# Kernel tuning notes

Hardware: AMD Instinct MI355X
Metric: run time of the kernel (lower is better)

## Reference

```python
import jax, jax.numpy as jnp
import numpy as np

W = 1022      # window_length (fft_length) -> 512 rfft bins
HOP = 256     # hop_length
F = 64        # frames
ORDER = 5     # butterworth order
WN = 0.5      # normalized cutoff (cutoff = fs/4)

# ---- Butterworth lowpass design (scipy.signal.butter equivalent, numpy only) ----
def _butter_lowpass(order, wn):
    m = np.arange(-order + 1, order, 2)
    p = -np.exp(1j * np.pi * m / (2 * order))        # analog prototype poles
    k = 1.0
    fs = 2.0
    warped = 2 * fs * np.tan(np.pi * wn / fs)        # pre-warp
    p = p * warped                                   # lp2lp
    k = k * warped ** order
    fs2 = 2 * fs                                     # bilinear
    pd = (fs2 + p) / (fs2 - p)
    zd = -np.ones(order)
    kd = k * np.real(1.0 / np.prod(fs2 - p))
    b = np.real(kd * np.poly(zd))
    a = np.real(np.poly(pd))
    return b / a[0], a / a[0]

_B_NP, _A_NP = _butter_lowpass(ORDER, WN)

def _lfilter_zi(b, a):
    n = max(len(a), len(b))
    A = np.zeros((n - 1, n - 1))
    A[0, :] = -a[1:]
    A[1:, :-1] = np.eye(n - 2)
    A = A.T
    Bv = b[1:] - a[1:] * b[0]
    return np.linalg.solve(np.eye(n - 1) - A, Bv)

_ZI_NP = _lfilter_zi(_B_NP, _A_NP)
PADLEN = 3 * max(len(_A_NP), len(_B_NP))  # scipy filtfilt default = 18

B_COEF = jnp.asarray(_B_NP, jnp.float32)
A_COEF = jnp.asarray(_A_NP, jnp.float32)
ZI = jnp.asarray(_ZI_NP, jnp.float32)

# ---- windows (tf.signal defaults: periodic Hann; inverse_stft_window_fn) ----
def _hann(n):
    return 0.5 - 0.5 * np.cos(2.0 * np.pi * np.arange(n) / n)

_FW = _hann(W)
_overlaps = -(-W // HOP)
_den = np.pad(_FW ** 2, (0, _overlaps * HOP - W))
_den = _den.reshape(_overlaps, HOP).sum(0)
_den = np.tile(_den, _overlaps)[:W]
SYN_WIN = jnp.asarray(_FW / _den, jnp.float32)   # synthesis window
FWD_WIN = jnp.asarray(_FW, jnp.float32)          # analysis window

_IDX = np.arange(F)[:, None] * HOP + np.arange(W)[None, :]  # [F, W]
T = HOP * (F - 1) + W  # 17150


def _lfilter(x, zi):
    # direct-form II transposed, batched over axis 0; x: [B,T], zi: [B,n]
    b0, b1, a1 = B_COEF[0], B_COEF[1:], A_COEF[1:]
    def step(z, xt):
        y = b0 * xt + z[:, 0]
        zs = jnp.concatenate([z[:, 1:], jnp.zeros_like(z[:, :1])], axis=1)
        z = zs + xt[:, None] * b1[None, :] - y[:, None] * a1[None, :]
        return z, y
    _, ys = jax.lax.scan(step, zi, x.T)
    return ys.T


def _filtfilt(x):
    # scipy.signal.filtfilt with padtype='odd', padlen=PADLEN
    left = 2.0 * x[:, :1] - x[:, PADLEN:0:-1]
    right = 2.0 * x[:, -1:] - x[:, -2:-PADLEN - 2:-1]
    xe = jnp.concatenate([left, x, right], axis=1)
    y = _lfilter(xe, ZI[None, :] * xe[:, :1])
    y = y[:, ::-1]
    y = _lfilter(y, ZI[None, :] * y[:, :1])
    y = y[:, ::-1]
    return y[:, PADLEN:-PADLEN]


def setup_inputs() -> dict:
    key = jax.random.key(0)
    x = jax.random.normal(key, (64, 512, F, 2), dtype=jnp.float32)
    return {"x": x}


def reference(x):
    bsz = x.shape[0]
    stfts = jax.lax.complex(x[..., 0], x[..., 1])          # [B,512,F]
    frames = jnp.transpose(stfts, (0, 2, 1))               # [B,F,512]
    # inverse STFT: irfft -> synthesis window -> overlap-add
    sig_frames = jnp.fft.irfft(frames, n=W, axis=-1) * SYN_WIN  # [B,F,W]
    signals = jnp.zeros((bsz, T), jnp.float32).at[:, _IDX.reshape(-1)].add(
        sig_frames.reshape(bsz, -1))                       # [B,T]
    filt = _filtfilt(signals)                              # [B,T]
    # forward STFT
    fr = filt[:, _IDX] * FWD_WIN                           # [B,F,W]
    S = jnp.fft.rfft(fr, n=W, axis=-1)                     # [B,F,512]
    S = jnp.transpose(S, (0, 2, 1))                        # [B,512,F]
    return jnp.stack([jnp.real(S), jnp.imag(S)], axis=-1)
```

## Files before the change

kernel.cpp:

```cpp
#include <hip/hip_runtime.h>
#include <cmath>
#include <complex>
#include <algorithm>

#define NW      1022
#define NB      64
#define TLEN    17150
#define PADL    18
#define LXLEN   17186
#define NFRAMES 4096
#define GK      1024
#define BS      4288
#define SPAN    4480

typedef __attribute__((ext_vector_type(8))) short short8;
typedef __attribute__((ext_vector_type(4))) float floatx4;

struct IirCoef {
  float b0,b1,b2,b3,b4,b5;
  float a1,a2,a3,a4,a5;
  float zi0,zi1,zi2,zi3,zi4;
};

static __device__ __forceinline__ ushort f2bf(float f) {
  uint32_t u = __builtin_bit_cast(uint32_t, f);
  uint32_t r = (u + 0x7FFFu + ((u >> 16) & 1u)) >> 16;
  return (ushort)r;
}

static __device__ __forceinline__ float phase_mod(int k, int t) {
  const float TPN = 6.2831853071795864769f / 1022.f;
  float kt = (float)(k * t);
  float q = floorf(kt * (1.0f / 1022.0f));
  float r = kt - q * 1022.0f;
  if (r < 0.f) r += 1022.f;
  if (r >= 1022.f) r -= 1022.f;
  return r * TPN;
}

__global__ __launch_bounds__(256) void prep(const float* __restrict__ x,
                                            ushort* __restrict__ BT1,
                                            ushort* __restrict__ BT2,
                                            ushort* __restrict__ A1) {
  __shared__ float tile[32][129];
  int bid = blockIdx.x;
  if (bid < 4096) {
    int idx = bid * 256 + threadIdx.x;
    int t = idx >> 10, kk = idx & 1023;
    int k = kk & 511;
    float val = 0.f;
    if (t < NW) {
      const float TPN = 6.2831853071795864769f / 1022.f;
      float fw = 0.5f - 0.5f * __cosf((float)t * TPN);
      float den = 0.f;
      int tm = t & 255;
      #pragma unroll
      for (int j = 0; j < 4; ++j) {
        int u = tm + (j << 8);
        if (u < NW) { float w = 0.5f - 0.5f * __cosf((float)u * TPN); den += w * w; }
      }
      float syn = fw / den;
      float arg = phase_mod(k, t);
      float scale = (k == 0 || k == 511) ? 1.f : 2.f;
      if (kk < 512) val = __cosf(arg) * scale * (1.f / 1022.f) * syn;
      else          val = (k == 0 || k == 511) ? 0.f
                          : -__sinf(arg) * scale * (1.f / 1022.f) * syn;
    }
    BT1[idx] = f2bf(val);
  } else if (bid < 8192) {
    int idx = (bid - 4096) * 256 + threadIdx.x;
    int kk = idx >> 10, t = idx & 1023;
    int k = kk & 511;
    float val = 0.f;
    if (t < NW) {
      const float TPN = 6.2831853071795864769f / 1022.f;
      float fw = 0.5f - 0.5f * __cosf((float)t * TPN);
      float arg = phase_mod(k, t);
      val = (kk < 512) ? fw * __cosf(arg) : -fw * __sinf(arg);
    }
    BT2[idx] = f2bf(val);
  } else {
    int tb = bid - 8192;
    int b  = tb >> 4;
    int k0 = (tb & 15) << 5;
    int tid = threadIdx.x;
    #pragma unroll
    for (int e = 0; e < 16; ++e) {
      int lin = tid + e * 256;
      int i = lin >> 7, c = lin & 127;
      tile[i][c] = x[(b * 512 + k0 + i) * 128 + c];
    }
    __syncthreads();
    #pragma unroll
    for (int e = 0; e < 16; ++e) {
      int lin = tid + e * 256;
      int c = lin >> 5, i = lin & 31;
      int f = c >> 1, ri = c & 1;
      A1[(b * 64 + f) * 1024 + ri * 512 + k0 + i] = f2bf(tile[i][c]);
    }
  }
}

#define GLOAD16(gsrc, ldst) \
  __builtin_amdgcn_global_load_lds( \
      (const __attribute__((address_space(1))) void*)(gsrc), \
      (__attribute__((address_space(3))) void*)(ldst), 16, 0, 0)

#define WAIT_VMCNT6()  __builtin_amdgcn_s_waitcnt(0xF76)
#define WAIT_VMCNT0()  __builtin_amdgcn_s_waitcnt(0xF70)

static __device__ __forceinline__ void gemm_compute64(
    const ushort* as, const ushort* bs, int arow, int brow, int g, int rx,
    floatx4 (&acc)[2][4]) {
  #pragma unroll
  for (int ks = 0; ks < 2; ++ks) {
    short8 af[2], bfr[4];
    const int chunk = ((ks << 2) + g) ^ rx;
    #pragma unroll
    for (int fm = 0; fm < 2; ++fm)
      af[fm] = *(const short8*)(as + (arow + fm * 16) * 64 + chunk * 8);
    #pragma unroll
    for (int fn = 0; fn < 4; ++fn)
      bfr[fn] = *(const short8*)(bs + (brow + fn * 16) * 64 + chunk * 8);
    #pragma unroll
    for (int fm = 0; fm < 2; ++fm)
      #pragma unroll
      for (int fn = 0; fn < 4; ++fn)
        acc[fm][fn] = __builtin_amdgcn_mfma_f32_16x16x32_bf16(
            af[fm], bfr[fn], acc[fm][fn], 0, 0, 0);
  }
}

__global__ __launch_bounds__(256, 2) void gemm1(
    const ushort* __restrict__ A, const ushort* __restrict__ Bt,
    float* __restrict__ C) {
  __shared__ __align__(16) ushort As[2][64 * 64];
  __shared__ __align__(16) ushort Bs[2][128 * 64];
  const int tid = threadIdx.x;
  const int wid = tid >> 6, lane = tid & 63;
  const int m0 = blockIdx.y * 64, n0 = blockIdx.x * 128;
  const int warp_m = wid >> 1, warp_n = wid & 1;

  floatx4 acc[2][4];
  #pragma unroll
  for (int i = 0; i < 2; ++i)
    #pragma unroll
    for (int j = 0; j < 4; ++j) acc[i][j] = (floatx4){0.f, 0.f, 0.f, 0.f};

  const int lr = lane >> 3, lc = lane & 7;
  const int swz = lc ^ lr;
  const ushort* aBase = A  + (size_t)(m0 + wid * 8 + lr) * GK + swz * 8;
  const ushort* bBase = Bt + (size_t)(n0 + wid * 8 + lr) * GK + swz * 8;

  const int lane15 = lane & 15;
  const int g = lane >> 4;
  const int rx = lane & 7;
  const int arow = warp_m * 32 + lane15;
  const int brow = warp_n * 64 + lane15;

#define STAGE_G1(buf, kk0) do { \
    _Pragma("unroll") \
    for (int p = 0; p < 2; ++p) \
      GLOAD16(aBase + (size_t)(p * 32) * GK + (kk0), &As[buf][(p * 32 + wid * 8) * 64]); \
    _Pragma("unroll") \
    for (int p = 0; p < 4; ++p) \
      GLOAD16(bBase + (size_t)(p * 32) * GK + (kk0), &Bs[buf][(p * 32 + wid * 8) * 64]); \
    } while (0)

  STAGE_G1(0, 0);
  for (int t = 0; t < 15; ++t) {
    STAGE_G1((t + 1) & 1, (t + 1) * 64);
    WAIT_VMCNT6();
    __builtin_amdgcn_s_barrier();
    __builtin_amdgcn_sched_barrier(0);
    gemm_compute64(&As[t & 1][0], &Bs[t & 1][0], arow, brow, g, rx, acc);
    __builtin_amdgcn_sched_barrier(0);
    __builtin_amdgcn_s_barrier();
  }
  WAIT_VMCNT0();
  __builtin_amdgcn_s_barrier();
  gemm_compute64(&As[1][0], &Bs[1][0], arow, brow, g, rx, acc);

  #pragma unroll
  for (int fm = 0; fm < 2; ++fm)
    #pragma unroll
    for (int fn = 0; fn < 4; ++fn)
      #pragma unroll
      for (int i = 0; i < 4; ++i) {
        int gm = m0 + warp_m * 32 + fm * 16 + g * 4 + i;
        int gn = n0 + warp_n * 64 + fn * 16 + lane15;
        C[(size_t)gm * 1024 + gn] = acc[fm][fn][i];
      }
#undef STAGE_G1
}

__global__ __launch_bounds__(256, 2) void gemm2(
    const ushort* __restrict__ Ftb, const ushort* __restrict__ Bt,
    float* __restrict__ out) {
  __shared__ __align__(16) ushort smem[2 * 64 * 64 + 2 * 128 * 64];
  ushort (*As)[64 * 64] = (ushort(*)[64 * 64])smem;
  ushort (*Bs)[128 * 64] = (ushort(*)[128 * 64])(smem + 2 * 64 * 64);
  float* CT = (float*)smem;
  const int tid = threadIdx.x;
  const int wid = tid >> 6, lane = tid & 63;
  const int by = blockIdx.y, bx = blockIdx.x;
  const int warp_m = wid >> 1, warp_n = wid & 1;

  floatx4 acc[2][4];
  #pragma unroll
  for (int i = 0; i < 2; ++i)
    #pragma unroll
    for (int j = 0; j < 4; ++j) acc[i][j] = (floatx4){0.f, 0.f, 0.f, 0.f};

  const int lr = lane >> 3, lc = lane & 7;
  const int swz = lc ^ lr;

  const ushort* aBase = Ftb + (size_t)by * TLEN + (wid * 8 + lr) * 256 + swz * 8;
  const ushort* bB0 = Bt + (size_t)(bx * 64 + wid * 8 + lr) * GK + swz * 8;

  const int lane15 = lane & 15;
  const int g = lane >> 4;
  const int rx = lane & 7;
  const int arow = warp_m * 32 + lane15;
  const int brow = warp_n * 64 + lane15;

#define STAGE_G2(buf, kk0) do { \
    _Pragma("unroll") \
    for (int p = 0; p < 2; ++p) \
      GLOAD16(aBase + (size_t)(p * 32) * 256 + (kk0), &As[buf][(p * 32 + wid * 8) * 64]); \
    _Pragma("unroll") \
    for (int p = 0; p < 4; ++p) { \
      size_t boff = (size_t)((p & 1) * 32 + (p >> 1) * 512) * GK; \
      GLOAD16(bB0 + boff + (kk0), &Bs[buf][(((p >> 1) * 64 + (p & 1) * 32) + wid * 8) * 64]); \
    } } while (0)

  STAGE_G2(0, 0);
  for (int t = 0; t < 15; ++t) {
    STAGE_G2((t + 1) & 1, (t + 1) * 64);
    WAIT_VMCNT6();
    __builtin_amdgcn_s_barrier();
    __builtin_amdgcn_sched_barrier(0);
    gemm_compute64(&As[t & 1][0], &Bs[t & 1][0], arow, brow, g, rx, acc);
    __builtin_amdgcn_sched_barrier(0);
    __builtin_amdgcn_s_barrier();
  }
  WAIT_VMCNT0();
  __builtin_amdgcn_s_barrier();
  gemm_compute64(&As[1][0], &Bs[1][0], arow, brow, g, rx, acc);

  __syncthreads();
  #pragma unroll
  for (int fm = 0; fm < 2; ++fm)
    #pragma unroll
    for (int fn = 0; fn < 4; ++fn)
      #pragma unroll
      for (int i = 0; i < 4; ++i) {
        int s    = warp_n * 64 + fn * 16 + lane15;
        int fcol = warp_m * 32 + fm * 16 + g * 4 + i;
        CT[s * 65 + fcol] = acc[fm][fn][i];
      }
  __syncthreads();
  #pragma unroll
  for (int e = 0; e < 8; ++e) {
    int it = tid + e * 256;
    int r = it >> 5, q = it & 31;
    float4 v;
    v.x = CT[r * 65 + 2 * q];
    v.y = CT[(64 + r) * 65 + 2 * q];
    v.z = CT[r * 65 + 2 * q + 1];
    v.w = CT[(64 + r) * 65 + 2 * q + 1];
    *(float4*)&out[((size_t)(by * 512 + bx * 64 + r)) * 128 + q * 4] = v;
  }
#undef STAGE_G2
}

#define SWZ(r) ((r) ^ (((r) >> 6) & 31))

static __device__ __forceinline__ float oa_sample(const float* __restrict__ frb,
                                                  int tau) {
  int fhi = tau >> 8;
  int flo = fhi - 3; if (flo < 0) flo = 0;
  if (fhi > 63) fhi = 63;
  float sum = 0.f;
  for (int f = flo; f <= fhi; ++f) {
    int off = tau - (f << 8);
    if (off < NW) sum += frb[(size_t)f * 1024 + off];
  }
  return sum;
}

#define IIR_STEP(x, y)                                   \
  float y = fmaf(cf.b0, (x), z0);                        \
  z0 = fmaf(-cf.a1, y, fmaf(cf.b1, (x), z1));            \
  z1 = fmaf(-cf.a2, y, fmaf(cf.b2, (x), z2));            \
  z2 = fmaf(-cf.a3, y, fmaf(cf.b3, (x), z3));            \
  z3 = fmaf(-cf.a4, y, fmaf(cf.b4, (x), z4));            \
  z4 = fmaf(-cf.a5, y, cf.b5 * (x));

__global__ __launch_bounds__(256) void oa_iir(const float* __restrict__ Fr,
                                              ushort* __restrict__ Ftb,
                                              IirCoef cf) {
  __shared__ float bufX[SPAN];
  __shared__ float bufY[SPAN];
  const int blk = blockIdx.x;
  const int b = blk >> 2, sp = blk & 3;
  const int lo = sp * BS;
  const int hi = (lo + BS < TLEN) ? lo + BS : TLEN;
  const int F0 = (sp == 0) ? 0 : lo + PADL;
  int F1 = hi + PADL + 128; if (F1 > LXLEN) F1 = LXLEN;
  const int XB = (sp == 0) ? 0 : F0 - 64;
  const int xspan = F1 - XB;
  const float* frb = Fr + (size_t)b * 64 * 1024;

  for (int rel = threadIdx.x; rel < xspan; rel += 256) {
    int p = XB + rel;
    float v;
    if (p < PADL)                 v = 2.f * oa_sample(frb, 0) - oa_sample(frb, PADL - p);
    else if (p < PADL + TLEN)     v = oa_sample(frb, p - PADL);
    else { int j = p - (PADL + TLEN);
           v = 2.f * oa_sample(frb, TLEN - 1) - oa_sample(frb, TLEN - 2 - j); }
    bufX[SWZ(rel)] = v;
  }
  __syncthreads();

  {
    int nch = (F1 - F0 + 63) >> 6;
    int c = threadIdx.x;
    if (c < nch) {
      int os = F0 + (c << 6);
      int oe = os + 64; if (oe > F1) oe = F1;
      float z0, z1, z2, z3, z4;
      int i;
      if (sp == 0 && c == 0) {
        float x0 = bufX[SWZ(0)];
        z0 = cf.zi0 * x0; z1 = cf.zi1 * x0; z2 = cf.zi2 * x0;
        z3 = cf.zi3 * x0; z4 = cf.zi4 * x0;
        i = 0;
      } else {
        z0 = z1 = z2 = z3 = z4 = 0.f;
        i = os - 64;
        #pragma unroll 4
        for (; i < os; ++i) { float x = bufX[SWZ(i - XB)]; IIR_STEP(x, y); (void)y; }
      }
      #pragma unroll 4
      for (; i < oe; ++i) {
        float x = bufX[SWZ(i - XB)];
        IIR_STEP(x, y);
        bufY[SWZ(i - XB)] = y;
      }
    }
  }
  __syncthreads();

  {
    const int R0 = TLEN + PADL - hi;
    const int R1 = LXLEN - lo - PADL;
    int k_lo = R0 >> 6, k_hi = (R1 - 1) >> 6;
    int k = k_lo + threadIdx.x;
    if (k <= k_hi) {
      int rs = k << 6;
      int re = rs + 64; if (re > R1) re = R1;
      float z0, z1, z2, z3, z4;
      int i;
      if (k == 0) {
        float x0 = bufY[SWZ(LXLEN - 1 - XB)];
        z0 = cf.zi0 * x0; z1 = cf.zi1 * x0; z2 = cf.zi2 * x0;
        z3 = cf.zi3 * x0; z4 = cf.zi4 * x0;
        i = 0;
      } else {
        z0 = z1 = z2 = z3 = z4 = 0.f;
        i = rs - 64;
        #pragma unroll 4
        for (; i < rs; ++i) { float x = bufY[SWZ(LXLEN - 1 - i - XB)]; IIR_STEP(x, y); (void)y; }
      }
      #pragma unroll 4
      for (; i < re; ++i) {
        float x = bufY[SWZ(LXLEN - 1 - i - XB)];
        IIR_STEP(x, y);
        if (i >= R0) bufX[SWZ(LXLEN - 1 - i - XB)] = y;
      }
    }
  }
  __syncthreads();

  for (int t = lo + threadIdx.x; t < hi; t += 256)
    Ftb[(size_t)b * TLEN + t] = f2bf(bufX[SWZ(t + PADL - XB)]);
  if (b == NB - 1 && sp == 3)
    for (int t = threadIdx.x; t < 1024; t += 256)
      Ftb[(size_t)NB * TLEN + t] = 0;
}

static void solve5(double M[5][5], double v[5], double outv[5]) {
  for (int col = 0; col < 5; ++col) {
    int piv = col;
    for (int r = col + 1; r < 5; ++r)
      if (std::fabs(M[r][col]) > std::fabs(M[piv][col])) piv = r;
    if (piv != col) {
      for (int c = 0; c < 5; ++c) std::swap(M[col][c], M[piv][c]);
      std::swap(v[col], v[piv]);
    }
    double d = M[col][col];
    for (int r = col + 1; r < 5; ++r) {
      double f = M[r][col] / d;
      for (int c = col; c < 5; ++c) M[r][c] -= f * M[col][c];
      v[r] -= f * v[col];
    }
  }
  for (int r = 4; r >= 0; --r) {
    double s = v[r];
    for (int c = r + 1; c < 5; ++c) s -= M[r][c] * outv[c];
    outv[r] = s / M[r][r];
  }
}

static IirCoef make_coef() {
  const double PI = 3.14159265358979323846;
  std::complex<double> p[5];
  for (int i = 0; i < 5; ++i) {
    double m = -4.0 + 2.0 * i;
    p[i] = -std::exp(std::complex<double>(0.0, PI * m / 10.0));
  }
  double fs = 2.0;
  double warped = 2.0 * fs * std::tan(PI * 0.5 / fs);
  for (int i = 0; i < 5; ++i) p[i] *= warped;
  double kgain = std::pow(warped, 5.0);
  double fs2 = 2.0 * fs;
  std::complex<double> pd[5], prod(1.0, 0.0);
  for (int i = 0; i < 5; ++i) {
    pd[i] = (fs2 + p[i]) / (fs2 - p[i]);
    prod *= (fs2 - p[i]);
  }
  double kd = kgain * std::real(1.0 / prod);
  double b[6] = {kd, 5 * kd, 10 * kd, 10 * kd, 5 * kd, kd};
  std::complex<double> c[6] = {{1,0},{0,0},{0,0},{0,0},{0,0},{0,0}};
  for (int i = 0; i < 5; ++i)
    for (int j = i + 1; j >= 1; --j)
      c[j] -= pd[i] * c[j - 1];
  double a[6]; for (int i = 0; i < 6; ++i) a[i] = c[i].real();
  double M[5][5], v[5];
  for (int r = 0; r < 5; ++r)
    for (int cc = 0; cc < 5; ++cc) {
      double Af = 0.0;
      if (cc == 0) Af = -a[r + 1];
      if (cc == r + 1) Af = 1.0;
      M[r][cc] = (r == cc ? 1.0 : 0.0) - Af;
    }
  for (int r = 0; r < 5; ++r) v[r] = b[r + 1] - a[r + 1] * b[0];
  double zi[5];
  solve5(M, v, zi);
  IirCoef cf;
  cf.b0 = (float)b[0]; cf.b1 = (float)b[1]; cf.b2 = (float)b[2];
  cf.b3 = (float)b[3]; cf.b4 = (float)b[4]; cf.b5 = (float)b[5];
  cf.a1 = (float)a[1]; cf.a2 = (float)a[2]; cf.a3 = (float)a[3];
  cf.a4 = (float)a[4]; cf.a5 = (float)a[5];
  cf.zi0 = (float)zi[0]; cf.zi1 = (float)zi[1]; cf.zi2 = (float)zi[2];
  cf.zi3 = (float)zi[3]; cf.zi4 = (float)zi[4];
  return cf;
}

extern "C" void kernel_launch(void* const* d_in, const int* in_sizes, int n_in,
                              void* d_out, int out_size, void* d_ws, size_t ws_size,
                              hipStream_t stream) {
  const float* x = (const float*)d_in[0];
  float* out = (float*)d_out;

  ushort* BT1 = (ushort*)d_ws;
  ushort* BT2 = BT1 + 1024 * 1024;
  ushort* A1  = BT2 + 1024 * 1024;
  ushort* Ftb = A1 + (size_t)NFRAMES * 1024;
  float*  Fr  = (float*)(Ftb + (size_t)NB * TLEN + 1024);
  size_t need = (size_t)((char*)(Fr + (size_t)NFRAMES * 1024) - (char*)d_ws);
  if (ws_size < need) return;

  IirCoef cf = make_coef();

  prep<<<9216, 256, 0, stream>>>(x, BT1, BT2, A1);
  gemm1<<<dim3(8, 64), 256, 0, stream>>>(A1, BT1, Fr);
  oa_iir<<<NB * 4, 256, 0, stream>>>(Fr, Ftb, cf);
  gemm2<<<dim3(8, 64), 256, 0, stream>>>(Ftb, BT2, out);
}
```

Measured before the change: 82.87 us.

## Exploit real-DFT even/odd symmetry to halve the K dimension of both GEMMs

The inverse DFT GEMM is split into separate cosine and sine products over 512 bins, producing U and V of half width. The symmetric frame sample is then rebuilt as U±V, with the synthesis window applied inside overlap-add. The forward DFT folds each frame into even and odd halves (a new fold kernel), so cosine and sine GEMMs run over K=512 instead of 1024, and the twiddle tables shrink fourfold. This cuts MFMA work and table generation, at the cost of an extra kernel launch, an extra bf16 round trip for the folded inputs, and more index arithmetic in the overlap-add.

```diff
diff --git a/kernel.cpp b/kernel.cpp
--- a/kernel.cpp
+++ b/kernel.cpp
@@ -9,7 +9,6 @@
 #define PADL    18
 #define LXLEN   17186
 #define NFRAMES 4096
-#define GK      1024
 #define BS      4288
 #define SPAN    4480
 
@@ -26,6 +25,9 @@
   uint32_t u = __builtin_bit_cast(uint32_t, f);
   uint32_t r = (u + 0x7FFFu + ((u >> 16) & 1u)) >> 16;
   return (ushort)r;
+}
+static __device__ __forceinline__ float bf2f(ushort u) {
+  return __builtin_bit_cast(float, (uint32_t)u << 16);
 }
 
 static __device__ __forceinline__ float phase_mod(int k, int t) {
@@ -39,18 +41,31 @@
 }
 
 __global__ __launch_bounds__(256) void prep(const float* __restrict__ x,
-                                            ushort* __restrict__ BT1,
-                                            ushort* __restrict__ BT2,
+                                            ushort* __restrict__ cb1,
+                                            ushort* __restrict__ sb1,
+                                            ushort* __restrict__ cb2,
+                                            ushort* __restrict__ sb2,
+                                            float* __restrict__ synT,
                                             ushort* __restrict__ A1) {
   __shared__ float tile[32][129];
+  const float TPN = 6.2831853071795864769f / 1022.f;
   int bid = blockIdx.x;
-  if (bid < 4096) {
+  if (bid < 1024) {
     int idx = bid * 256 + threadIdx.x;
-    int t = idx >> 10, kk = idx & 1023;
-    int k = kk & 511;
-    float val = 0.f;
-    if (t < NW) {
-      const float TPN = 6.2831853071795864769f / 1022.f;
+    int t = idx >> 9, k = idx & 511;
+    float arg = phase_mod(k, t);
+    float s = ((k == 0 || k == 511) ? 1.f : 2.f) * (1.f / 1022.f);
+    cb1[idx] = f2bf(__cosf(arg) * s);
+    sb1[idx] = f2bf(-__sinf(arg) * s);
+  } else if (bid < 2048) {
+    int idx = (bid - 1024) * 256 + threadIdx.x;
+    int k = idx >> 9, t = idx & 511;
+    float fw = 0.5f - 0.5f * __cosf((float)t * TPN);
+    float arg = phase_mod(k, t);
+    cb2[idx] = f2bf(fw * __cosf(arg));
+    sb2[idx] = f2bf(-fw * __sinf(arg));
+  } else if (bid == 2048) {
+    for (int t = threadIdx.x; t < NW; t += 256) {
       float fw = 0.5f - 0.5f * __cosf((float)t * TPN);
       float den = 0.f;
       int tm = t & 255;
@@ -59,28 +74,10 @@
         int u = tm + (j << 8);
         if (u < NW) { float w = 0.5f - 0.5f * __cosf((float)u * TPN); den += w * w; }
       }
-      float syn = fw / den;
-      float arg = phase_mod(k, t);
-      float scale = (k == 0 || k == 511) ? 1.f : 2.f;
-      if (kk < 512) val = __cosf(arg) * scale * (1.f / 1022.f) * syn;
-      else          val = (k == 0 || k == 511) ? 0.f
-                          : -__sinf(arg) * scale * (1.f / 1022.f) * syn;
-    }
-    BT1[idx] = f2bf(val);
-  } else if (bid < 8192) {
-    int idx = (bid - 4096) * 256 + threadIdx.x;
-    int kk = idx >> 10, t = idx & 1023;
-    int k = kk & 511;
-    float val = 0.f;
-    if (t < NW) {
-      const float TPN = 6.2831853071795864769f / 1022.f;
-      float fw = 0.5f - 0.5f * __cosf((float)t * TPN);
-      float arg = phase_mod(k, t);
-      val = (kk < 512) ? fw * __cosf(arg) : -fw * __sinf(arg);
-    }
-    BT2[idx] = f2bf(val);
+      synT[t] = fw / den;
+    }
   } else {
-    int tb = bid - 8192;
+    int tb = bid - 2049;
     int b  = tb >> 4;
     int k0 = (tb & 15) << 5;
     int tid = threadIdx.x;
@@ -106,6 +103,7 @@
       (const __attribute__((address_space(1))) void*)(gsrc), \
       (__attribute__((address_space(3))) void*)(ldst), 16, 0, 0)
 
+#define WAIT_VMCNT8()  __builtin_amdgcn_s_waitcnt(0xF78)
 #define WAIT_VMCNT6()  __builtin_amdgcn_s_waitcnt(0xF76)
 #define WAIT_VMCNT0()  __builtin_amdgcn_s_waitcnt(0xF70)
 
@@ -132,14 +130,18 @@
 }
 
 __global__ __launch_bounds__(256, 2) void gemm1(
-    const ushort* __restrict__ A, const ushort* __restrict__ Bt,
-    float* __restrict__ C) {
+    const ushort* __restrict__ A1, const ushort* __restrict__ cb1,
+    const ushort* __restrict__ sb1, float* __restrict__ U,
+    float* __restrict__ V) {
   __shared__ __align__(16) ushort As[2][64 * 64];
   __shared__ __align__(16) ushort Bs[2][128 * 64];
   const int tid = threadIdx.x;
   const int wid = tid >> 6, lane = tid & 63;
-  const int m0 = blockIdx.y * 64, n0 = blockIdx.x * 128;
+  const int uv = blockIdx.x >> 2, nb = blockIdx.x & 3;
+  const int m0 = blockIdx.y * 64, n0 = nb * 128;
   const int warp_m = wid >> 1, warp_n = wid & 1;
+  const ushort* Bt = uv ? sb1 : cb1;
+  float* C = uv ? V : U;
 
   floatx4 acc[2][4];
   #pragma unroll
@@ -149,8 +151,8 @@
 
   const int lr = lane >> 3, lc = lane & 7;
   const int swz = lc ^ lr;
-  const ushort* aBase = A  + (size_t)(m0 + wid * 8 + lr) * GK + swz * 8;
-  const ushort* bBase = Bt + (size_t)(n0 + wid * 8 + lr) * GK + swz * 8;
+  const ushort* aBase = A1 + (size_t)(m0 + wid * 8 + lr) * 1024 + uv * 512 + swz * 8;
+  const ushort* bBase = Bt + (size_t)(n0 + wid * 8 + lr) * 512 + swz * 8;
 
   const int lane15 = lane & 15;
   const int g = lane >> 4;
@@ -161,14 +163,14 @@
 #define STAGE_G1(buf, kk0) do { \
     _Pragma("unroll") \
     for (int p = 0; p < 2; ++p) \
-      GLOAD16(aBase + (size_t)(p * 32) * GK + (kk0), &As[buf][(p * 32 + wid * 8) * 64]); \
+      GLOAD16(aBase + (size_t)(p * 32) * 1024 + (kk0), &As[buf][(p * 32 + wid * 8) * 64]); \
     _Pragma("unroll") \
     for (int p = 0; p < 4; ++p) \
-      GLOAD16(bBase + (size_t)(p * 32) * GK + (kk0), &Bs[buf][(p * 32 + wid * 8) * 64]); \
+      GLOAD16(bBase + (size_t)(p * 32) * 512 + (kk0), &Bs[buf][(p * 32 + wid * 8) * 64]); \
     } while (0)
 
   STAGE_G1(0, 0);
-  for (int t = 0; t < 15; ++t) {
+  for (int t = 0; t < 7; ++t) {
     STAGE_G1((t + 1) & 1, (t + 1) * 64);
     WAIT_VMCNT6();
     __builtin_amdgcn_s_barrier();
@@ -189,22 +191,20 @@
       for (int i = 0; i < 4; ++i) {
         int gm = m0 + warp_m * 32 + fm * 16 + g * 4 + i;
         int gn = n0 + warp_n * 64 + fn * 16 + lane15;
-        C[(size_t)gm * 1024 + gn] = acc[fm][fn][i];
+        C[(size_t)gm * 512 + gn] = acc[fm][fn][i];
       }
 #undef STAGE_G1
 }
 
 __global__ __launch_bounds__(256, 2) void gemm2(
-    const ushort* __restrict__ Ftb, const ushort* __restrict__ Bt,
+    const ushort* __restrict__ Ae, const ushort* __restrict__ Ao,
+    const ushort* __restrict__ cb2, const ushort* __restrict__ sb2,
     float* __restrict__ out) {
-  __shared__ __align__(16) ushort smem[2 * 64 * 64 + 2 * 128 * 64];
-  ushort (*As)[64 * 64] = (ushort(*)[64 * 64])smem;
-  ushort (*Bs)[128 * 64] = (ushort(*)[128 * 64])(smem + 2 * 64 * 64);
-  float* CT = (float*)smem;
+  __shared__ __align__(16) ushort smem[32768];
   const int tid = threadIdx.x;
   const int wid = tid >> 6, lane = tid & 63;
-  const int by = blockIdx.y, bx = blockIdx.x;
-  const int warp_m = wid >> 1, warp_n = wid & 1;
+  const int kx = blockIdx.x, by = blockIdx.y;
+  const int warp_m = wid >> 1, half = wid & 1;
 
   floatx4 acc[2][4];
   #pragma unroll
@@ -214,69 +214,87 @@
 
   const int lr = lane >> 3, lc = lane & 7;
   const int swz = lc ^ lr;
-
-  const ushort* aBase = Ftb + (size_t)by * TLEN + (wid * 8 + lr) * 256 + swz * 8;
-  const ushort* bB0 = Bt + (size_t)(bx * 64 + wid * 8 + lr) * GK + swz * 8;
+  const size_t arow_g = (size_t)(by * 64 + wid * 8 + lr) * 512 + swz * 8;
+  const size_t brow_g = (size_t)(kx * 64 + wid * 8 + lr) * 512 + swz * 8;
+  const ushort* aeB = Ae + arow_g;
+  const ushort* aoB = Ao + arow_g;
+  const ushort* cbB = cb2 + brow_g;
+  const ushort* sbB = sb2 + brow_g;
 
   const int lane15 = lane & 15;
   const int g = lane >> 4;
   const int rx = lane & 7;
   const int arow = warp_m * 32 + lane15;
-  const int brow = warp_n * 64 + lane15;
 
 #define STAGE_G2(buf, kk0) do { \
     _Pragma("unroll") \
-    for (int p = 0; p < 2; ++p) \
-      GLOAD16(aBase + (size_t)(p * 32) * 256 + (kk0), &As[buf][(p * 32 + wid * 8) * 64]); \
-    _Pragma("unroll") \
-    for (int p = 0; p < 4; ++p) { \
-      size_t boff = (size_t)((p & 1) * 32 + (p >> 1) * 512) * GK; \
-      GLOAD16(bB0 + boff + (kk0), &Bs[buf][(((p >> 1) * 64 + (p & 1) * 32) + wid * 8) * 64]); \
+    for (int p = 0; p < 2; ++p) { \
+      int ld = (p * 32 + wid * 8) * 64; \
+      size_t go = (size_t)(p * 32) * 512 + (kk0); \
+      GLOAD16(aeB + go, &smem[(buf) * 2 * 4096 + ld]); \
+      GLOAD16(aoB + go, &smem[((buf) * 2 + 1) * 4096 + ld]); \
+      GLOAD16(cbB + go, &smem[16384 + (buf) * 2 * 4096 + ld]); \
+      GLOAD16(sbB + go, &smem[16384 + ((buf) * 2 + 1) * 4096 + ld]); \
     } } while (0)
 
   STAGE_G2(0, 0);
-  for (int t = 0; t < 15; ++t) {
+  for (int t = 0; t < 7; ++t) {
     STAGE_G2((t + 1) & 1, (t + 1) * 64);
-    WAIT_VMCNT6();
+    WAIT_VMCNT8();
     __builtin_amdgcn_s_barrier();
     __builtin_amdgcn_sched_barrier(0);
-    gemm_compute64(&As[t & 1][0], &Bs[t & 1][0], arow, brow, g, rx, acc);
+    gemm_compute64(&smem[((t & 1) * 2 + half) * 4096],
+                   &smem[16384 + ((t & 1) * 2 + half) * 4096],
+                   arow, lane15, g, rx, acc);
     __builtin_amdgcn_sched_barrier(0);
     __builtin_amdgcn_s_barrier();
   }
   WAIT_VMCNT0();
   __builtin_amdgcn_s_barrier();
-  gemm_compute64(&As[1][0], &Bs[1][0], arow, brow, g, rx, acc);
+  gemm_compute64(&smem[(2 + half) * 4096], &smem[16384 + (2 + half) * 4096],
+                 arow, lane15, g, rx, acc);
 
   __syncthreads();
+  float* CT = (float*)smem;
   #pragma unroll
   for (int fm = 0; fm < 2; ++fm)
     #pragma unroll
     for (int fn = 0; fn < 4; ++fn)
       #pragma unroll
       for (int i = 0; i < 4; ++i) {
-        int s    = warp_n * 64 + fn * 16 + lane15;
-        int fcol = warp_m * 32 + fm * 16 + g * 4 + i;
-        CT[s * 65 + fcol] = acc[fm][fn][i];
+        int f = warp_m * 32 + fm * 16 + g * 4 + i;
+        int k = fn * 16 + lane15;
+        CT[k * 132 + f * 2 + half] = acc[fm][fn][i];
       }
   __syncthreads();
   #pragma unroll
   for (int e = 0; e < 8; ++e) {
     int it = tid + e * 256;
     int r = it >> 5, q = it & 31;
-    float4 v;
-    v.x = CT[r * 65 + 2 * q];
-    v.y = CT[(64 + r) * 65 + 2 * q];
-    v.z = CT[r * 65 + 2 * q + 1];
-    v.w = CT[(64 + r) * 65 + 2 * q + 1];
-    *(float4*)&out[((size_t)(by * 512 + bx * 64 + r)) * 128 + q * 4] = v;
+    float4 v = *(float4*)&CT[r * 132 + q * 4];
+    *(float4*)&out[((size_t)(by * 512 + kx * 64 + r)) * 128 + q * 4] = v;
   }
 #undef STAGE_G2
 }
 
+__global__ __launch_bounds__(256) void fold(const ushort* __restrict__ Ftb,
+                                            ushort* __restrict__ Ae,
+                                            ushort* __restrict__ Ao) {
+  int idx = blockIdx.x * 256 + threadIdx.x;
+  int fid = idx >> 9, t = idx & 511;
+  int b = fid >> 6, f = fid & 63;
+  const ushort* base = Ftb + (size_t)b * TLEN + (f << 8);
+  float s1 = bf2f(base[t]);
+  float s2 = (t == 511) ? 0.f : bf2f(base[1022 - t]);
+  Ae[idx] = f2bf(s1 + s2);
+  Ao[idx] = f2bf(s1 - s2);
+}
+
 #define SWZ(r) ((r) ^ (((r) >> 6) & 31))
 
-static __device__ __forceinline__ float oa_sample(const float* __restrict__ frb,
+static __device__ __forceinline__ float oa_sample(const float* __restrict__ ub,
+                                                  const float* __restrict__ vb,
+                                                  const float* __restrict__ synl,
                                                   int tau) {
   int fhi = tau >> 8;
   int flo = fhi - 3; if (flo < 0) flo = 0;
@@ -284,7 +302,12 @@
   float sum = 0.f;
   for (int f = flo; f <= fhi; ++f) {
     int off = tau - (f << 8);
-    if (off < NW) sum += frb[(size_t)f * 1024 + off];
+    if (off < NW) {
+      int o2 = (off < 512) ? off : 1022 - off;
+      float u = ub[f * 512 + o2], v = vb[f * 512 + o2];
+      float y = (off < 512) ? u + v : u - v;
+      sum += synl[off] * y;
+    }
   }
   return sum;
 }
@@ -297,11 +320,14 @@
   z3 = fmaf(-cf.a4, y, fmaf(cf.b4, (x), z4));            \
   z4 = fmaf(-cf.a5, y, cf.b5 * (x));
 
-__global__ __launch_bounds__(256) void oa_iir(const float* __restrict__ Fr,
+__global__ __launch_bounds__(256) void oa_iir(const float* __restrict__ U,
+                                              const float* __restrict__ V,
+                                              const float* __restrict__ synT,
                                               ushort* __restrict__ Ftb,
                                               IirCoef cf) {
   __shared__ float bufX[SPAN];
   __shared__ float bufY[SPAN];
+  __shared__ float synl[NW];
   const int blk = blockIdx.x;
   const int b = blk >> 2, sp = blk & 3;
   const int lo = sp * BS;
@@ -310,15 +336,23 @@
   int F1 = hi + PADL + 128; if (F1 > LXLEN) F1 = LXLEN;
   const int XB = (sp == 0) ? 0 : F0 - 64;
   const int xspan = F1 - XB;
-  const float* frb = Fr + (size_t)b * 64 * 1024;
+  const float* ub = U + (size_t)(b * 64) * 512;
+  const float* vb = V + (size_t)(b * 64) * 512;
+
+  for (int i = threadIdx.x; i < NW; i += 256) synl[i] = synT[i];
+  __syncthreads();
 
   for (int rel = threadIdx.x; rel < xspan; rel += 256) {
     int p = XB + rel;
     float v;
-    if (p < PADL)                 v = 2.f * oa_sample(frb, 0) - oa_sample(frb, PADL - p);
-    else if (p < PADL + TLEN)     v = oa_sample(frb, p - PADL);
-    else { int j = p - (PADL + TLEN);
-           v = 2.f * oa_sample(frb, TLEN - 1) - oa_sample(frb, TLEN - 2 - j); }
+    if (p < PADL)
+      v = 2.f * oa_sample(ub, vb, synl, 0) - oa_sample(ub, vb, synl, PADL - p);
+    else if (p < PADL + TLEN)
+      v = oa_sample(ub, vb, synl, p - PADL);
+    else {
+      int j = p - (PADL + TLEN);
+      v = 2.f * oa_sample(ub, vb, synl, TLEN - 1) - oa_sample(ub, vb, synl, TLEN - 2 - j);
+    }
     bufX[SWZ(rel)] = v;
   }
   __syncthreads();
@@ -464,18 +498,25 @@
   const float* x = (const float*)d_in[0];
   float* out = (float*)d_out;
 
-  ushort* BT1 = (ushort*)d_ws;
-  ushort* BT2 = BT1 + 1024 * 1024;
-  ushort* A1  = BT2 + 1024 * 1024;
+  ushort* cb1 = (ushort*)d_ws;
+  ushort* sb1 = cb1 + 262144;
+  ushort* cb2 = sb1 + 262144;
+  ushort* sb2 = cb2 + 262144;
+  float*  synT = (float*)(sb2 + 262144);
+  ushort* A1  = (ushort*)(synT + 1024);
   ushort* Ftb = A1 + (size_t)NFRAMES * 1024;
-  float*  Fr  = (float*)(Ftb + (size_t)NB * TLEN + 1024);
-  size_t need = (size_t)((char*)(Fr + (size_t)NFRAMES * 1024) - (char*)d_ws);
+  ushort* Ae  = Ftb + (size_t)NB * TLEN + 1024;
+  ushort* Ao  = Ae + (size_t)NFRAMES * 512;
+  float*  U   = (float*)(Ao + (size_t)NFRAMES * 512);
+  float*  V   = U + (size_t)NFRAMES * 512;
+  size_t need = (size_t)((char*)(V + (size_t)NFRAMES * 512) - (char*)d_ws);
   if (ws_size < need) return;
 
   IirCoef cf = make_coef();
 
-  prep<<<9216, 256, 0, stream>>>(x, BT1, BT2, A1);
-  gemm1<<<dim3(8, 64), 256, 0, stream>>>(A1, BT1, Fr);
-  oa_iir<<<NB * 4, 256, 0, stream>>>(Fr, Ftb, cf);
-  gemm2<<<dim3(8, 64), 256, 0, stream>>>(Ftb, BT2, out);
-}
+  prep<<<3073, 256, 0, stream>>>(x, cb1, sb1, cb2, sb2, synT, A1);
+  gemm1<<<dim3(8, 64), 256, 0, stream>>>(A1, cb1, sb1, U, V);
+  oa_iir<<<NB * 4, 256, 0, stream>>>(U, V, synT, Ftb, cf);
+  fold<<<8192, 256, 0, stream>>>(Ftb, Ae, Ao);
+  gemm2<<<dim3(8, 64), 256, 0, stream>>>(Ae, Ao, cb2, sb2, out);
+}
```

After: 80.98 us. 2.3% less time.
